# Kernel tuning notes

Hardware: AMD Instinct MI355X
Metric: run time of the kernel (lower is better)

Reference implementation:

```python
import jax, jax.numpy as jnp
import numpy as np
from jax import lax

DEPTH, STACKS = 8, 2
C, SK, OUT = 64, 256, 256          # res_channels, skip_channels, out_channels
NB = DEPTH * STACKS                 # 16 blocks
DILS = [2 ** i for i in range(DEPTH)] * STACKS


def causal_conv(x, w, dil):
    # x: [B,C,T], w: [2C,C,2]; causal: left-pad by dil, kernel size 2 dilated
    return lax.conv_general_dilated(
        x, w, window_strides=(1,), padding=[(dil, 0)], rhs_dilation=(dil,),
        dimension_numbers=('NCH', 'OIH', 'NCH'))


def conv1x1(x, w):
    # x: [B,c_in,T], w: [c_out,c_in]
    return jnp.einsum('oc,bct->bot', w, x)


def setup_inputs() -> dict:
    key = jax.random.key(0)
    ks = jax.random.split(key, 8)
    B, T = 4, 8192
    x = jax.random.randint(ks[0], (B, T), 0, 256)
    h = jax.random.normal(ks[1], (B, NB * 2 * C, T), dtype=jnp.float32)
    embed = jax.random.normal(ks[2], (256, C), dtype=jnp.float32) * 0.1
    w_conv = jax.random.normal(ks[3], (NB, 2 * C, C, 2), dtype=jnp.float32) * 0.08
    w_res = jax.random.normal(ks[4], (NB, C, C), dtype=jnp.float32) * 0.08
    w_skip = jax.random.normal(ks[5], (NB, SK, C), dtype=jnp.float32) * 0.08
    w_out1 = jax.random.normal(ks[6], (OUT, SK), dtype=jnp.float32) * 0.05
    w_out2 = jax.random.normal(ks[7], (OUT, OUT), dtype=jnp.float32) * 0.05
    return {'x': x, 'h': h, 'embed': embed, 'w_conv': w_conv,
            'w_res': w_res, 'w_skip': w_skip, 'w_out1': w_out1, 'w_out2': w_out2}


def reference(x, h, embed, w_conv, w_res, w_skip, w_out1, w_out2):
    out = embed[x].transpose(0, 2, 1)          # [B,C,T]
    hs = jnp.split(h, NB, axis=1)              # NB chunks of [B,2C,T]
    skip = None
    for i in range(NB):
        g = causal_conv(out, w_conv[i], DILS[i]) + hs[i]   # [B,2C,T]
        z = jnp.tanh(g[:, :C]) * jax.nn.sigmoid(g[:, C:])  # gated activation
        s = conv1x1(z, w_skip[i])                          # [B,SK,T]
        skip = s if skip is None else skip + s
        if i < NB - 1:  # last block has return_residual=False (skip only)
            out = out + conv1x1(z, w_res[i])
    y = jax.nn.relu(skip)
    y = jax.nn.relu(conv1x1(y, w_out1))
    return conv1x1(y, w_out2)                  # [B,OUT,T]
```

## Files before the change

### kernel.cpp

```cpp
#include <hip/hip_runtime.h>

#define NB 16
#define TT 8192
#define Bb 4

typedef __attribute__((ext_vector_type(8))) short short8;
typedef __attribute__((ext_vector_type(16))) float f32x16;

__device__ __forceinline__ unsigned short bf16_rn(float f) {
  unsigned int u = __float_as_uint(f);
  u += 0x7FFF + ((u >> 16) & 1);
  return (unsigned short)(u >> 16);
}
__device__ __forceinline__ unsigned int pack2(float a, float b) {
  return (unsigned int)bf16_rn(a) | ((unsigned int)bf16_rn(b) << 16);
}
__device__ __forceinline__ int kpos(int k) {
  int g = (k >> 2) & 1;
  int e = (k & 3) + 4 * (k >> 3);
  return g * 8 + e;
}
__device__ __forceinline__ int kinv(int p) {
  int g = p >> 3, e = p & 7;
  return (e & 3) + 4 * g + 8 * (e >> 2);
}

#define WINRD(base, r, off)                                                    \
  (*(const short8*)((char*)(base) +                                            \
      (((unsigned int)((r) * 128 + (off) * 2)) ^                               \
       ((unsigned int)(((r) & 7) << 4)))))

__global__ __launch_bounds__(256) void prep_weights(
    const float* __restrict__ wconv, const float* __restrict__ wres,
    const float* __restrict__ wsk, const float* __restrict__ w1,
    const float* __restrict__ w2, short* __restrict__ dwc,
    short* __restrict__ dwr, short* __restrict__ dws,
    short* __restrict__ dw1, short* __restrict__ dw2)
{
  int i = blockIdx.x * 256 + threadIdx.x;
  if (i < 262144) {
    int k = kinv(i & 15);
    int ic = (i & 48) | k;
    int oc = (i >> 6) & 127;
    int tap = (i >> 13) & 1;
    int blk = i >> 14;
    dwc[i] = (short)bf16_rn(wconv[(((blk * 128 + oc) * 64 + ic) << 1) | tap]);
    return;
  }
  int j = i - 262144;
  if (j < 65536) { dwr[j] = (short)bf16_rn(wres[(j & ~15) | kinv(j & 15)]); return; }
  j -= 65536;
  if (j < 262144) { dws[j] = (short)bf16_rn(wsk[(j & ~15) | kinv(j & 15)]); return; }
  j -= 262144;
  if (j < 65536) { dw1[j] = (short)bf16_rn(w1[(j & ~15) | kinv(j & 15)]); return; }
  j -= 65536;
  if (j < 65536) { dw2[j] = (short)bf16_rn(w2[(j & ~15) | kinv(j & 15)]); return; }
}

template <int DIL, int FIRST, int LAST>
__global__ __launch_bounds__(256, 3) void block_kernel(
    const float* __restrict__ rin, float* __restrict__ rout,
    const int* __restrict__ x, const float* __restrict__ embed,
    const float* __restrict__ h, const short* __restrict__ wc,
    const short* __restrict__ wr, unsigned short* __restrict__ zg,
    int blk)
{
  __shared__ short win[2][(32 + DIL) * 64];
  __shared__ float rs[2][32 * 64];
  __shared__ short zl[2][32 * 64];

  const int b = blockIdx.y;
  const int tile = threadIdx.x >> 7;
  const int htid = threadIdx.x & 127;
  const int t0 = (blockIdx.x * 2 + tile) * 32;
  const int lane = htid & 63, wv = htid >> 6;
  const int l31 = lane & 31, hi = lane >> 5;

  short* winT = win[tile];
  float* rsT = rs[tile];
  short* zlT = zl[tile];

  const int tcol = t0 + l31;
  f32x16 aA, aS;
  const float* hb = h + ((size_t)b * 2048 + (size_t)blk * 128) * TT;
#pragma unroll
  for (int r = 0; r < 16; ++r) {
    int row = (r & 3) + 4 * hi + 8 * (r >> 2) + 32 * wv;
    aA[r] = hb[(size_t)row * TT + tcol];
    aS[r] = hb[(size_t)(row + 64) * TT + tcol];
  }

  if (FIRST) {
    const int* xb = x + b * TT;
#pragma unroll
    for (int it = 0; it < 8; ++it) {
      int u = it * 128 + htid;
      int cpair = u & 31, t = u >> 5;
      int c0 = cpair * 2;
      int xi = xb[t0 + t];
      float v0 = embed[(size_t)xi * 64 + c0];
      float v1 = embed[(size_t)xi * 64 + c0 + 1];
      rsT[t * 64 + c0] = v0;
      rsT[t * 64 + c0 + 1] = v1;
      int p0 = (c0 & 48) | kpos(c0 & 15);
      int w = DIL + t;
      unsigned int byte = (unsigned int)(w * 128 + p0 * 2) ^
                          (unsigned int)((w & 7) << 4);
      *(unsigned int*)((char*)winT + byte) = pack2(v0, v1);
    }
    if (htid < 32) {
      int c0 = htid * 2;
      float v0 = 0.f, v1 = 0.f;
      if (t0 > 0) {
        int xi = xb[t0 - 1];
        v0 = embed[(size_t)xi * 64 + c0];
        v1 = embed[(size_t)xi * 64 + c0 + 1];
      }
      int p0 = (c0 & 48) | kpos(c0 & 15);
      unsigned int byte = (unsigned int)(p0 * 2);
      *(unsigned int*)((char*)winT + byte) = pack2(v0, v1);
    }
  } else {
    const float* rbase = rin + (size_t)b * TT * 64;
#pragma unroll
    for (int it = 0; it < 8; ++it) {
      int u = it * 128 + htid;
      int cpair = u & 31, t = u >> 5;
      int c0 = cpair * 2;
      float2 f = *(const float2*)(rbase + (size_t)(t0 + t) * 64 + c0);
      rsT[t * 64 + c0] = f.x;
      rsT[t * 64 + c0 + 1] = f.y;
      int p0 = (c0 & 48) | kpos(c0 & 15);
      int w = DIL + t;
      unsigned int byte = (unsigned int)(w * 128 + p0 * 2) ^
                          (unsigned int)((w & 7) << 4);
      *(unsigned int*)((char*)winT + byte) = pack2(f.x, f.y);
    }
#pragma unroll
    for (int it = 0; it < (DIL * 32 + 127) / 128; ++it) {
      int u = it * 128 + htid;
      if (DIL * 32 >= 128 || u < DIL * 32) {
        int cpair = u & 31, w = u >> 5;
        int c0 = cpair * 2;
        int gt = t0 - DIL + w;
        float2 f = {0.f, 0.f};
        if (gt >= 0) f = *(const float2*)(rbase + (size_t)gt * 64 + c0);
        int p0 = (c0 & 48) | kpos(c0 & 15);
        unsigned int byte = (unsigned int)(w * 128 + p0 * 2) ^
                            (unsigned int)((w & 7) << 4);
        *(unsigned int*)((char*)winT + byte) = pack2(f.x, f.y);
      }
    }
  }
  __syncthreads();

  const short* wA0 = wc + (size_t)blk * 16384 + (32 * wv + l31) * 64;
  const short* wA1 = wA0 + 8192;
  const int r1 = DIL + l31;
  const int r0 = l31;
#pragma unroll
  for (int ks = 0; ks < 4; ++ks) {
    int off = ks * 16 + 8 * hi;
    short8 b1 = WINRD(winT, r1, off);
    short8 b0 = WINRD(winT, r0, off);
    short8 a0t = *(const short8*)(wA0 + off);
    short8 a1t = *(const short8*)(wA1 + off);
    short8 a0s = *(const short8*)(wA0 + 4096 + off);
    short8 a1s = *(const short8*)(wA1 + 4096 + off);
    aA = __builtin_amdgcn_mfma_f32_32x32x16_bf16(a0t, b0, aA, 0, 0, 0);
    aA = __builtin_amdgcn_mfma_f32_32x32x16_bf16(a1t, b1, aA, 0, 0, 0);
    aS = __builtin_amdgcn_mfma_f32_32x32x16_bf16(a0s, b0, aS, 0, 0, 0);
    aS = __builtin_amdgcn_mfma_f32_32x32x16_bf16(a1s, b1, aS, 0, 0, 0);
  }

#pragma unroll
  for (int r = 0; r < 16; r += 2) {
    int ic0 = (r & 3) + 4 * hi + 8 * (r >> 2) + 32 * wv;
    float z0 = (1.f - 2.f / (__expf(2.f * aA[r]) + 1.f)) *
               (1.f / (1.f + __expf(-aS[r])));
    float z1 = (1.f - 2.f / (__expf(2.f * aA[r + 1]) + 1.f)) *
               (1.f / (1.f + __expf(-aS[r + 1])));
    int p = (ic0 & ~15) | kpos(ic0 & 15);
    int tloc = l31;
    unsigned int byte = (unsigned int)(tloc * 128 + p * 2) ^
                        (unsigned int)((tloc & 7) << 4);
    *(unsigned int*)((char*)zlT + byte) = pack2(z0, z1);
  }
  __syncthreads();

  {
    unsigned short* zb = zg + ((size_t)(blk * Bb + b) * TT + t0) * 64;
#pragma unroll
    for (int it = 0; it < 8; ++it) {
      int u = it * 128 + htid;
      int p2 = u & 31, t = u >> 5;
      unsigned int byte = (unsigned int)(t * 128 + p2 * 4) ^
                          (unsigned int)((t & 7) << 4);
      unsigned int v = *(const unsigned int*)((char*)zlT + byte);
      *(unsigned int*)(zb + (size_t)t * 64 + p2 * 2) = v;
    }
  }

  if (!LAST) {
    const int trow = l31;
    f32x16 ar = {};
    const short* wrb = wr + (size_t)blk * 4096 + (wv * 32 + l31) * 64;
#pragma unroll
    for (int ks = 0; ks < 4; ++ks) {
      int off = ks * 16 + 8 * hi;
      short8 az = WINRD(zlT, trow, off);
      short8 bw = *(const short8*)(wrb + off);
      ar = __builtin_amdgcn_mfma_f32_32x32x16_bf16(az, bw, ar, 0, 0, 0);
    }
    float* obase = rout + (size_t)b * TT * 64;
    int oc = wv * 32 + l31;
#pragma unroll
    for (int r = 0; r < 16; ++r) {
      int t = (r & 3) + 4 * hi + 8 * (r >> 2);
      obase[(size_t)(t0 + t) * 64 + oc] = rsT[t * 64 + oc] + ar[r];
    }
  }
}

__global__ __launch_bounds__(256) void head_kernel(
    const unsigned short* __restrict__ zg, const short* __restrict__ wsk,
    const short* __restrict__ w1, const short* __restrict__ w2,
    float* __restrict__ out)
{
  __shared__ short zbuf[2][32 * 64];
  __shared__ short yb[32 * 256];
  __shared__ short y2b[32 * 256];

  const int b = blockIdx.y;
  const int t0 = blockIdx.x * 32;
  const int tid = threadIdx.x;
  const int lane = tid & 63, wv = tid >> 6;
  const int l31 = lane & 31, hi = lane >> 5;

  {
#pragma unroll
    for (int it = 0; it < 4; ++it) {
      int u = it * 256 + tid;
      int p2 = u & 31, t = u >> 5;
      unsigned int v = *(const unsigned int*)(zg +
          ((size_t)(0 * Bb + b) * TT + t0 + t) * 64 + p2 * 2);
      unsigned int byte = (unsigned int)(t * 128 + p2 * 4) ^
                          (unsigned int)((t & 7) << 4);
      *(unsigned int*)((char*)zbuf[0] + byte) = v;
    }
  }

  f32x16 acc0 = {}, acc1 = {};
  const short* wsb0 = wsk + (wv * 32 + l31) * 64;
  const short* wsb1 = wsk + ((wv + 4) * 32 + l31) * 64;

  for (int blk = 0; blk < NB; ++blk) {
    __syncthreads();
    if (blk < NB - 1) {
#pragma unroll
      for (int it = 0; it < 4; ++it) {
        int u = it * 256 + tid;
        int p2 = u & 31, t = u >> 5;
        unsigned int v = *(const unsigned int*)(zg +
            ((size_t)((blk + 1) * Bb + b) * TT + t0 + t) * 64 + p2 * 2);
        unsigned int byte = (unsigned int)(t * 128 + p2 * 4) ^
                            (unsigned int)((t & 7) << 4);
        *(unsigned int*)((char*)zbuf[(blk + 1) & 1] + byte) = v;
      }
    }
    const short* zb = zbuf[blk & 1];
#pragma unroll
    for (int ks = 0; ks < 4; ++ks) {
      int off = ks * 16 + 8 * hi;
      short8 bw0 = *(const short8*)(wsb0 + (size_t)blk * 16384 + off);
      short8 bw1 = *(const short8*)(wsb1 + (size_t)blk * 16384 + off);
      short8 az = WINRD(zb, l31, off);
      acc0 = __builtin_amdgcn_mfma_f32_32x32x16_bf16(az, bw0, acc0, 0, 0, 0);
      acc1 = __builtin_amdgcn_mfma_f32_32x32x16_bf16(az, bw1, acc1, 0, 0, 0);
    }
  }

  {
    int sk0 = wv * 32 + l31;
    int sk1 = sk0 + 128;
    int p0 = (sk0 & 0xF0) | kpos(sk0 & 15);
    int p1 = (sk1 & 0xF0) | kpos(sk1 & 15);
#pragma unroll
    for (int r = 0; r < 16; ++r) {
      int dt = (r & 3) + 4 * hi + 8 * (r >> 2);
      unsigned int b0 = (unsigned int)(dt * 512 + p0 * 2) ^
                        (unsigned int)((dt & 7) << 4);
      unsigned int b1 = (unsigned int)(dt * 512 + p1 * 2) ^
                        (unsigned int)((dt & 7) << 4);
      *(short*)((char*)yb + b0) = (short)bf16_rn(fmaxf(acc0[r], 0.f));
      *(short*)((char*)yb + b1) = (short)bf16_rn(fmaxf(acc1[r], 0.f));
    }
  }
  __syncthreads();

#pragma unroll
  for (int ot = 0; ot < 2; ++ot) {
    const short* w1r = w1 + ((wv + 4 * ot) * 32 + l31) * 256;
    const int trow = l31;
    f32x16 acc = {};
#pragma unroll
    for (int ks = 0; ks < 16; ++ks) {
      int off = ks * 16 + 8 * hi;
      short8 by = *(const short8*)((char*)yb +
          ((unsigned int)(trow * 512 + off * 2) ^ (unsigned int)((trow & 7) << 4)));
      short8 aw = *(const short8*)(w1r + off);
      acc = __builtin_amdgcn_mfma_f32_32x32x16_bf16(aw, by, acc, 0, 0, 0);
    }
#pragma unroll
    for (int r = 0; r < 16; r += 2) {
      int o0 = (wv + 4 * ot) * 32 + (r & 3) + 4 * hi + 8 * (r >> 2);
      unsigned int v = (unsigned int)bf16_rn(fmaxf(acc[r], 0.f)) |
                       ((unsigned int)bf16_rn(fmaxf(acc[r + 1], 0.f)) << 16);
      int p = (o0 & 0xF0) | kpos(o0 & 15);
      unsigned int byte = (unsigned int)(trow * 512 + p * 2) ^
                          (unsigned int)((trow & 7) << 4);
      *(unsigned int*)((char*)y2b + byte) = v;
    }
  }
  __syncthreads();

  {
    float* ob = out + (size_t)b * 256 * TT;
#pragma unroll
    for (int ot = 0; ot < 2; ++ot) {
      const short* w2r = w2 + ((wv + 4 * ot) * 32 + l31) * 256;
      const int trow = l31;
      f32x16 acc = {};
#pragma unroll
      for (int ks = 0; ks < 16; ++ks) {
        int off = ks * 16 + 8 * hi;
        short8 by = *(const short8*)((char*)y2b +
            ((unsigned int)(trow * 512 + off * 2) ^ (unsigned int)((trow & 7) << 4)));
        short8 aw = *(const short8*)(w2r + off);
        acc = __builtin_amdgcn_mfma_f32_32x32x16_bf16(aw, by, acc, 0, 0, 0);
      }
#pragma unroll
      for (int r = 0; r < 16; ++r) {
        int oc = (wv + 4 * ot) * 32 + (r & 3) + 4 * hi + 8 * (r >> 2);
        ob[(size_t)oc * TT + t0 + trow] = acc[r];
      }
    }
  }
}

extern "C" void kernel_launch(void* const* d_in, const int* in_sizes, int n_in,
                              void* d_out, int out_size, void* d_ws, size_t ws_size,
                              hipStream_t stream)
{
  const int* x = (const int*)d_in[0];
  const float* h = (const float*)d_in[1];
  const float* embed = (const float*)d_in[2];
  const float* w_conv = (const float*)d_in[3];
  const float* w_res = (const float*)d_in[4];
  const float* w_skip = (const float*)d_in[5];
  const float* w_out1 = (const float*)d_in[6];
  const float* w_out2 = (const float*)d_in[7];
  float* out = (float*)d_out;

  char* ws = (char*)d_ws;
  float* r0 = (float*)ws;
  float* r1 = (float*)(ws + (size_t)(8 << 20));
  unsigned short* zg = (unsigned short*)(ws + (size_t)(16 << 20));
  short* dwc = (short*)(ws + (size_t)(80 << 20));
  short* dwr = dwc + 262144;
  short* dws = dwr + 65536;
  short* dw1 = dws + 262144;
  short* dw2 = dw1 + 65536;

  prep_weights<<<2816, 256, 0, stream>>>(w_conv, w_res, w_skip, w_out1, w_out2,
                                         dwc, dwr, dws, dw1, dw2);

  float* rf[2] = {r0, r1};
  const dim3 grid(TT / 64, Bb);

#define LAUNCH_BLK(DIL, FIRST, LAST, i)                                        \
  block_kernel<DIL, FIRST, LAST><<<grid, 256, 0, stream>>>(                    \
      rf[(i) & 1], rf[((i) + 1) & 1], x, embed, h, dwc, dwr, zg, (i))

  LAUNCH_BLK(1, 1, 0, 0);
  LAUNCH_BLK(2, 0, 0, 1);
  LAUNCH_BLK(4, 0, 0, 2);
  LAUNCH_BLK(8, 0, 0, 3);
  LAUNCH_BLK(16, 0, 0, 4);
  LAUNCH_BLK(32, 0, 0, 5);
  LAUNCH_BLK(64, 0, 0, 6);
  LAUNCH_BLK(128, 0, 0, 7);
  LAUNCH_BLK(1, 0, 0, 8);
  LAUNCH_BLK(2, 0, 0, 9);
  LAUNCH_BLK(4, 0, 0, 10);
  LAUNCH_BLK(8, 0, 0, 11);
  LAUNCH_BLK(16, 0, 0, 12);
  LAUNCH_BLK(32, 0, 0, 13);
  LAUNCH_BLK(64, 0, 0, 14);
  LAUNCH_BLK(128, 0, 1, 15);
#undef LAUNCH_BLK

  head_kernel<<<dim3(TT / 32, Bb), 256, 0, stream>>>(zg, dws, dw1, dw2, out);
}
```

Measured before the change: 365.0 us.

## Stage h tile through LDS with float4 loads and widen residual loads

The h-bias accumulator init no longer does strided scalar global loads straight into the MFMA layout. It now loads the 128x32 h tile with coalesced float4 reads into a new shared buffer and then reads it back in accumulator order. Residual-stream loads are widened from float2 to float4, with two packed bf16 stores each. The launch-bounds occupancy hint of 3 is dropped. The extra 32KB of LDS per block may lower occupancy.

```diff
diff --git a/kernel.cpp b/kernel.cpp
--- a/kernel.cpp
+++ b/kernel.cpp
@@ -58,7 +58,7 @@
 }
 
 template <int DIL, int FIRST, int LAST>
-__global__ __launch_bounds__(256, 3) void block_kernel(
+__global__ __launch_bounds__(256) void block_kernel(
     const float* __restrict__ rin, float* __restrict__ rout,
     const int* __restrict__ x, const float* __restrict__ embed,
     const float* __restrict__ h, const short* __restrict__ wc,
@@ -68,6 +68,7 @@
   __shared__ short win[2][(32 + DIL) * 64];
   __shared__ float rs[2][32 * 64];
   __shared__ short zl[2][32 * 64];
+  __shared__ float hl[2][128 * 32];
 
   const int b = blockIdx.y;
   const int tile = threadIdx.x >> 7;
@@ -79,15 +80,17 @@
   short* winT = win[tile];
   float* rsT = rs[tile];
   short* zlT = zl[tile];
-
-  const int tcol = t0 + l31;
-  f32x16 aA, aS;
-  const float* hb = h + ((size_t)b * 2048 + (size_t)blk * 128) * TT;
-#pragma unroll
-  for (int r = 0; r < 16; ++r) {
-    int row = (r & 3) + 4 * hi + 8 * (r >> 2) + 32 * wv;
-    aA[r] = hb[(size_t)row * TT + tcol];
-    aS[r] = hb[(size_t)(row + 64) * TT + tcol];
+  float* hlT = hl[tile];
+
+  {
+    const float* hb = h + ((size_t)b * 2048 + (size_t)blk * 128) * TT + t0;
+#pragma unroll
+    for (int it = 0; it < 8; ++it) {
+      int u = it * 128 + htid;
+      int q = u & 7, row = u >> 3;
+      float4 v = *(const float4*)(hb + (size_t)row * TT + q * 4);
+      *(float4*)(hlT + row * 32 + q * 4) = v;
+    }
   }
 
   if (FIRST) {
@@ -123,36 +126,49 @@
   } else {
     const float* rbase = rin + (size_t)b * TT * 64;
 #pragma unroll
-    for (int it = 0; it < 8; ++it) {
+    for (int it = 0; it < 4; ++it) {
       int u = it * 128 + htid;
-      int cpair = u & 31, t = u >> 5;
-      int c0 = cpair * 2;
-      float2 f = *(const float2*)(rbase + (size_t)(t0 + t) * 64 + c0);
-      rsT[t * 64 + c0] = f.x;
-      rsT[t * 64 + c0 + 1] = f.y;
-      int p0 = (c0 & 48) | kpos(c0 & 15);
+      int q = u & 15, t = u >> 4;
+      int c0 = q * 4;
+      float4 f = *(const float4*)(rbase + (size_t)(t0 + t) * 64 + c0);
+      *(float4*)(rsT + t * 64 + c0) = f;
       int w = DIL + t;
-      unsigned int byte = (unsigned int)(w * 128 + p0 * 2) ^
-                          (unsigned int)((w & 7) << 4);
-      *(unsigned int*)((char*)winT + byte) = pack2(f.x, f.y);
-    }
-#pragma unroll
-    for (int it = 0; it < (DIL * 32 + 127) / 128; ++it) {
+      int pa = (c0 & 48) | kpos(c0 & 15);
+      int pb = ((c0 + 2) & 48) | kpos((c0 + 2) & 15);
+      unsigned int sw = (unsigned int)((w & 7) << 4);
+      *(unsigned int*)((char*)winT + (((unsigned int)(w * 128 + pa * 2)) ^ sw)) =
+          pack2(f.x, f.y);
+      *(unsigned int*)((char*)winT + (((unsigned int)(w * 128 + pb * 2)) ^ sw)) =
+          pack2(f.z, f.w);
+    }
+#pragma unroll
+    for (int it = 0; it < (DIL * 16 + 127) / 128; ++it) {
       int u = it * 128 + htid;
-      if (DIL * 32 >= 128 || u < DIL * 32) {
-        int cpair = u & 31, w = u >> 5;
-        int c0 = cpair * 2;
+      if (DIL * 16 >= 128 || u < DIL * 16) {
+        int q = u & 15, w = u >> 4;
+        int c0 = q * 4;
         int gt = t0 - DIL + w;
-        float2 f = {0.f, 0.f};
-        if (gt >= 0) f = *(const float2*)(rbase + (size_t)gt * 64 + c0);
-        int p0 = (c0 & 48) | kpos(c0 & 15);
-        unsigned int byte = (unsigned int)(w * 128 + p0 * 2) ^
-                            (unsigned int)((w & 7) << 4);
-        *(unsigned int*)((char*)winT + byte) = pack2(f.x, f.y);
+        float4 f = {0.f, 0.f, 0.f, 0.f};
+        if (gt >= 0) f = *(const float4*)(rbase + (size_t)gt * 64 + c0);
+        int pa = (c0 & 48) | kpos(c0 & 15);
+        int pb = ((c0 + 2) & 48) | kpos((c0 + 2) & 15);
+        unsigned int sw = (unsigned int)((w & 7) << 4);
+        *(unsigned int*)((char*)winT + (((unsigned int)(w * 128 + pa * 2)) ^ sw)) =
+            pack2(f.x, f.y);
+        *(unsigned int*)((char*)winT + (((unsigned int)(w * 128 + pb * 2)) ^ sw)) =
+            pack2(f.z, f.w);
       }
     }
   }
   __syncthreads();
+
+  f32x16 aA, aS;
+#pragma unroll
+  for (int r = 0; r < 16; ++r) {
+    int row = (r & 3) + 4 * hi + 8 * (r >> 2) + 32 * wv;
+    aA[r] = hlT[row * 32 + l31];
+    aS[r] = hlT[(row + 64) * 32 + l31];
+  }
 
   const short* wA0 = wc + (size_t)blk * 16384 + (32 * wv + l31) * 64;
   const short* wA1 = wA0 + 8192;
```

Measured after the change: 368.6 us. No clear change (+1.0%).

## Store residual stream in bf16 with permuted channel layout between blocks

Applied to the files above, without the earlier changes.

The residual buffer passed between the 16 block kernels changes from fp32 to bf16, stored in the same permuted channel order the MFMA window expects. Loads become straight 16-byte vector copies into the LDS window, and the fp32 shared copy of the residual is dropped; the residual add now reads the bf16 value back from the window. This halves residual global traffic and cuts LDS use and conversion work. The cost is that rounding the residual to bf16 after every block accumulates error across the 16 blocks. The launch_bounds occupancy hint is also removed.

```diff
diff --git a/kernel.cpp b/kernel.cpp
--- a/kernel.cpp
+++ b/kernel.cpp
@@ -11,6 +11,9 @@
   unsigned int u = __float_as_uint(f);
   u += 0x7FFF + ((u >> 16) & 1);
   return (unsigned short)(u >> 16);
+}
+__device__ __forceinline__ float bf16_to_f(unsigned short s) {
+  return __uint_as_float(((unsigned int)s) << 16);
 }
 __device__ __forceinline__ unsigned int pack2(float a, float b) {
   return (unsigned int)bf16_rn(a) | ((unsigned int)bf16_rn(b) << 16);
@@ -58,15 +61,14 @@
 }
 
 template <int DIL, int FIRST, int LAST>
-__global__ __launch_bounds__(256, 3) void block_kernel(
-    const float* __restrict__ rin, float* __restrict__ rout,
+__global__ __launch_bounds__(256) void block_kernel(
+    const unsigned short* __restrict__ rin16, unsigned short* __restrict__ rout16,
     const int* __restrict__ x, const float* __restrict__ embed,
     const float* __restrict__ h, const short* __restrict__ wc,
     const short* __restrict__ wr, unsigned short* __restrict__ zg,
     int blk)
 {
   __shared__ short win[2][(32 + DIL) * 64];
-  __shared__ float rs[2][32 * 64];
   __shared__ short zl[2][32 * 64];
 
   const int b = blockIdx.y;
@@ -77,7 +79,6 @@
   const int l31 = lane & 31, hi = lane >> 5;
 
   short* winT = win[tile];
-  float* rsT = rs[tile];
   short* zlT = zl[tile];
 
   const int tcol = t0 + l31;
@@ -100,8 +101,6 @@
       int xi = xb[t0 + t];
       float v0 = embed[(size_t)xi * 64 + c0];
       float v1 = embed[(size_t)xi * 64 + c0 + 1];
-      rsT[t * 64 + c0] = v0;
-      rsT[t * 64 + c0 + 1] = v1;
       int p0 = (c0 & 48) | kpos(c0 & 15);
       int w = DIL + t;
       unsigned int byte = (unsigned int)(w * 128 + p0 * 2) ^
@@ -121,35 +120,25 @@
       *(unsigned int*)((char*)winT + byte) = pack2(v0, v1);
     }
   } else {
-    const float* rbase = rin + (size_t)b * TT * 64;
-#pragma unroll
-    for (int it = 0; it < 8; ++it) {
+    const unsigned short* rb16 = rin16 + (size_t)b * TT * 64;
+#pragma unroll
+    for (int it = 0; it < 2; ++it) {
       int u = it * 128 + htid;
-      int cpair = u & 31, t = u >> 5;
-      int c0 = cpair * 2;
-      float2 f = *(const float2*)(rbase + (size_t)(t0 + t) * 64 + c0);
-      rsT[t * 64 + c0] = f.x;
-      rsT[t * 64 + c0 + 1] = f.y;
-      int p0 = (c0 & 48) | kpos(c0 & 15);
+      int q = u & 7, t = u >> 3;
+      short8 v = *(const short8*)(rb16 + (size_t)(t0 + t) * 64 + q * 8);
       int w = DIL + t;
-      unsigned int byte = (unsigned int)(w * 128 + p0 * 2) ^
+      unsigned int byte = (unsigned int)(w * 128 + q * 16) ^
                           (unsigned int)((w & 7) << 4);
-      *(unsigned int*)((char*)winT + byte) = pack2(f.x, f.y);
-    }
-#pragma unroll
-    for (int it = 0; it < (DIL * 32 + 127) / 128; ++it) {
-      int u = it * 128 + htid;
-      if (DIL * 32 >= 128 || u < DIL * 32) {
-        int cpair = u & 31, w = u >> 5;
-        int c0 = cpair * 2;
-        int gt = t0 - DIL + w;
-        float2 f = {0.f, 0.f};
-        if (gt >= 0) f = *(const float2*)(rbase + (size_t)gt * 64 + c0);
-        int p0 = (c0 & 48) | kpos(c0 & 15);
-        unsigned int byte = (unsigned int)(w * 128 + p0 * 2) ^
-                            (unsigned int)((w & 7) << 4);
-        *(unsigned int*)((char*)winT + byte) = pack2(f.x, f.y);
-      }
+      *(short8*)((char*)winT + byte) = v;
+    }
+    for (int u = htid; u < DIL * 8; u += 128) {
+      int q = u & 7, w = u >> 3;
+      int gt = t0 - DIL + w;
+      short8 v = {};
+      if (gt >= 0) v = *(const short8*)(rb16 + (size_t)gt * 64 + q * 8);
+      unsigned int byte = (unsigned int)(w * 128 + q * 16) ^
+                          (unsigned int)((w & 7) << 4);
+      *(short8*)((char*)winT + byte) = v;
     }
   }
   __syncthreads();
@@ -212,12 +201,16 @@
       short8 bw = *(const short8*)(wrb + off);
       ar = __builtin_amdgcn_mfma_f32_32x32x16_bf16(az, bw, ar, 0, 0, 0);
     }
-    float* obase = rout + (size_t)b * TT * 64;
+    unsigned short* obase = rout16 + (size_t)b * TT * 64;
     int oc = wv * 32 + l31;
+    int ocp = (oc & 48) | kpos(oc & 15);
 #pragma unroll
     for (int r = 0; r < 16; ++r) {
       int t = (r & 3) + 4 * hi + 8 * (r >> 2);
-      obase[(size_t)(t0 + t) * 64 + oc] = rsT[t * 64 + oc] + ar[r];
+      int w = DIL + t;
+      unsigned short ov = *(const unsigned short*)((char*)winT +
+          (((unsigned int)(w * 128 + ocp * 2)) ^ ((unsigned int)((w & 7) << 4))));
+      obase[(size_t)(t0 + t) * 64 + ocp] = bf16_rn(bf16_to_f(ov) + ar[r]);
     }
   }
 }
@@ -363,10 +356,10 @@
   float* out = (float*)d_out;
 
   char* ws = (char*)d_ws;
-  float* r0 = (float*)ws;
-  float* r1 = (float*)(ws + (size_t)(8 << 20));
-  unsigned short* zg = (unsigned short*)(ws + (size_t)(16 << 20));
-  short* dwc = (short*)(ws + (size_t)(80 << 20));
+  unsigned short* r0 = (unsigned short*)ws;
+  unsigned short* r1 = (unsigned short*)(ws + (size_t)(4 << 20));
+  unsigned short* zg = (unsigned short*)(ws + (size_t)(8 << 20));
+  short* dwc = (short*)(ws + (size_t)(72 << 20));
   short* dwr = dwc + 262144;
   short* dws = dwr + 65536;
   short* dw1 = dws + 262144;
@@ -375,7 +368,7 @@
   prep_weights<<<2816, 256, 0, stream>>>(w_conv, w_res, w_skip, w_out1, w_out2,
                                          dwc, dwr, dws, dw1, dw2);
 
-  float* rf[2] = {r0, r1};
+  unsigned short* rf[2] = {r0, r1};
   const dim3 grid(TT / 64, Bb);
 
 #define LAUNCH_BLK(DIL, FIRST, LAST, i)                                        \
```

Result: faster. 323.7 us (median of 2 runs) (-11.3%).
